# Kernel optimization log

Hardware: AMD Instinct MI355X
Metric: run time of the kernel (lower is better)

Reference implementation:

```python
import jax, jax.numpy as jnp
import numpy as np

B = 262144
NUM_PLAYERS = 450
EMBED = 8


def _lin(x, w, b):
    return x @ w + b


def setup_inputs() -> dict:
    key = jax.random.key(0)
    ks = jax.random.split(key, 32)
    # state: 73 continuous features + 5 player ids stored as floats
    cont = jax.random.normal(ks[0], (B, 73), dtype=jnp.float32)
    pids = jax.random.randint(ks[1], (B, 5), 0, NUM_PLAYERS).astype(jnp.float32)
    state = jnp.concatenate([cont, pids], axis=1)

    def w(k, shape, fan_in):
        return jax.random.normal(k, shape, dtype=jnp.float32) * (2.0 / fan_in) ** 0.5

    base_in = 13 + EMBED + 32      # ctx(21) + pooled defender phi(32) = 53
    pass_in = 32 + base_in         # tm_phi(32) + base(53) = 85? no: 32+53=85 -> wait
    pass_in = 32 + (13 + EMBED) + 32  # tm_phi + ctx + def_pooled = 32+21+32 = 85
    # Match torch: pass_input = 32 + ctx_dim + 32 where ctx_dim = 13+embed = 21 -> 85?
    # torch: ctx_dim = 13 + embed_dim = 21; base_input = ctx_dim + 32 = 53; pass_input = 32 + ctx_dim + 32 = 85.
    # BUT forward concatenates [tm_phi, ctx, def_pooled] = 32 + 21 + 32 = 85. Consistent.
    pass_in = 85
    return {
        "state": state,
        "emb": jax.random.normal(ks[2], (NUM_PLAYERS, EMBED), dtype=jnp.float32),
        "wd1": w(ks[3], (4, 32), 4),   "bd1": jnp.zeros((32,), jnp.float32),
        "wd2": w(ks[4], (32, 32), 32), "bd2": jnp.zeros((32,), jnp.float32),
        "wt1": w(ks[5], (10 + EMBED, 32), 18), "bt1": jnp.zeros((32,), jnp.float32),
        "wt2": w(ks[6], (32, 32), 32),         "bt2": jnp.zeros((32,), jnp.float32),
        "wv1": w(ks[7], (base_in, 64), base_in), "bv1": jnp.zeros((64,), jnp.float32),
        "wv2": w(ks[8], (64, 32), 64),           "bv2": jnp.zeros((32,), jnp.float32),
        "wv3": w(ks[9], (32, 1), 32),            "bv3": jnp.zeros((1,), jnp.float32),
        "ws1": w(ks[10], (base_in, 32), base_in), "bs1": jnp.zeros((32,), jnp.float32),
        "ws2": w(ks[11], (32, 1), 32),            "bs2": jnp.zeros((1,), jnp.float32),
        "wp1": w(ks[12], (pass_in, 64), pass_in), "bp1": jnp.zeros((64,), jnp.float32),
        "wp2": w(ks[13], (64, 16), 64),           "bp2": jnp.zeros((16,), jnp.float32),
        "wp3": w(ks[14], (16, 1), 16),            "bp3": jnp.zeros((1,), jnp.float32),
    }


def reference(state, emb, wd1, bd1, wd2, bd2, wt1, bt1, wt2, bt2,
              wv1, bv1, wv2, bv2, wv3, bv3, ws1, bs1, ws2, bs2,
              wp1, bp1, wp2, bp2, wp3, bp3):
    b = state.shape[0]
    context = state[:, :11]
    tm_open = state[:, 11:15]
    tm_fg = state[:, 15:19]
    tm_dist = state[:, 19:23]
    def_pos = state[:, 23:33].reshape(b, 5, 2)
    tm_pos = state[:, 33:41].reshape(b, 4, 2)
    bh_vel = state[:, 41:43]
    def_vel = state[:, 43:53].reshape(b, 5, 2)
    tm_vel = state[:, 53:61].reshape(b, 4, 2)
    tm_lane_min = state[:, 61:65]
    tm_corridor = state[:, 65:69]
    tm_pass_dist = state[:, 69:73]

    pids = jnp.clip(state[:, 73:78].astype(jnp.int32), 0, NUM_PLAYERS - 1)
    bh_embed = emb[pids[:, 0]]            # [b, E]
    tm_embeds = emb[pids[:, 1:5]]         # [b, 4, E]

    # batched defender phi over 5 entities: [b,5,4] -> [b,5,32]
    d_feat = jnp.concatenate([def_pos, def_vel], axis=-1)
    d_h = jax.nn.relu(jax.nn.relu(d_feat @ wd1 + bd1) @ wd2 + bd2)
    def_pooled = d_h.mean(axis=1)         # [b, 32]

    ctx = jnp.concatenate([context, bh_vel, bh_embed], axis=1)   # [b, 21]
    base = jnp.concatenate([ctx, def_pooled], axis=1)            # [b, 53]

    value = jax.nn.relu(jax.nn.relu(base @ wv1 + bv1) @ wv2 + bv2) @ wv3 + bv3  # [b,1]
    a_shoot = jax.nn.relu(base @ ws1 + bs1) @ ws2 + bs2                          # [b,1]

    # batched teammate phi over 4 entities: [b,4,18] -> [b,4,32]
    t_feat = jnp.concatenate([
        tm_pos, tm_vel,
        tm_open[:, :, None], tm_fg[:, :, None], tm_dist[:, :, None],
        tm_lane_min[:, :, None], tm_corridor[:, :, None], tm_pass_dist[:, :, None],
        tm_embeds,
    ], axis=-1)
    tm_phi = jax.nn.relu(jax.nn.relu(t_feat @ wt1 + bt1) @ wt2 + bt2)  # [b,4,32]

    base_b = jnp.broadcast_to(base[:, None, :], (b, 4, base.shape[1]))
    p_in = jnp.concatenate([tm_phi, base_b], axis=-1)                   # [b,4,85]
    a_pass = (jax.nn.relu(jax.nn.relu(p_in @ wp1 + bp1) @ wp2 + bp2) @ wp3 + bp3)[..., 0]  # [b,4]
    a_pass = a_pass - a_pass.mean(axis=1, keepdims=True)

    q_shoot = value + a_shoot          # [b,1]
    q_passes = value + a_pass          # [b,4]
    return jnp.concatenate([q_shoot, q_passes], axis=1)
```

## Files before the change

kernel.cpp:

```cpp
#include <hip/hip_runtime.h>
#include <hip/hip_bf16.h>

#define THREADS 512

typedef short bf16x8 __attribute__((ext_vector_type(8)));
typedef float f32x4 __attribute__((ext_vector_type(4)));

union FragU { unsigned u[4]; bf16x8 v; };

__device__ __forceinline__ void split8(const float* x, FragU& hi, FragU& lo) {
#pragma unroll
    for (int i = 0; i < 4; ++i) {
        float a = x[2 * i], b = x[2 * i + 1];
        __hip_bfloat162 h2 = __float22bfloat162_rn(make_float2(a, b));
        float ra = __bfloat162float(h2.x), rb = __bfloat162float(h2.y);
        __hip_bfloat162 l2 = __float22bfloat162_rn(make_float2(a - ra, b - rb));
        unsigned hu, lu;
        __builtin_memcpy(&hu, &h2, 4);
        __builtin_memcpy(&lu, &l2, 4);
        hi.u[i] = hu; lo.u[i] = lu;
    }
}

__device__ __forceinline__ f32x4 mm3(const FragU& ah, const FragU& al,
                                     const FragU& bh, const FragU& bl, f32x4 acc) {
    acc = __builtin_amdgcn_mfma_f32_16x16x32_bf16(al.v, bh.v, acc, 0, 0, 0);
    acc = __builtin_amdgcn_mfma_f32_16x16x32_bf16(ah.v, bl.v, acc, 0, 0, 0);
    acc = __builtin_amdgcn_mfma_f32_16x16x32_bf16(ah.v, bh.v, acc, 0, 0, 0);
    return acc;
}

__device__ __forceinline__ void load_pair(const uint4* __restrict__ ws, int pair, int lane,
                                          FragU& hi, FragU& lo) {
    uint4 a = ws[pair * 128 + lane];
    uint4 b = ws[pair * 128 + 64 + lane];
    hi.u[0] = a.x; hi.u[1] = a.y; hi.u[2] = a.z; hi.u[3] = a.w;
    lo.u[0] = b.x; lo.u[1] = b.y; lo.u[2] = b.z; lo.u[3] = b.w;
}

__device__ __forceinline__ void buildA(const float* buf, int stride, int m, int kf, int lane,
                                       FragU& hi, FragU& lo) {
    const float* p = buf + (m * 16 + (lane & 15)) * stride + kf * 32 + ((lane >> 4) * 8);
    float x[8];
    *reinterpret_cast<float4*>(&x[0]) = *reinterpret_cast<const float4*>(p);
    *reinterpret_cast<float4*>(&x[4]) = *reinterpret_cast<const float4*>(p + 4);
    split8(x, hi, lo);
}

__device__ __forceinline__ void storeC(float* buf, int stride, int m, int nf, int lane, f32x4 c) {
    float* p = buf + (((lane >> 4) * 4) + m * 16) * stride + nf * 16 + (lane & 15);
    p[0] = c[0]; p[stride] = c[1]; p[2 * stride] = c[2]; p[3 * stride] = c[3];
}

#define PB_D2  0
#define PB_T1  2
#define PB_T2  4
#define PB_P1T 6
#define PB_P1B 10
#define PB_P2  18
#define PB_V1  20
#define PB_V2  28
#define PB_S1  32
#define WS_BYTES (36 * 2048)

__global__ __launch_bounds__(64)
void prep_weights(const float* __restrict__ wd2, const float* __restrict__ wt1,
                  const float* __restrict__ wt2, const float* __restrict__ wp1,
                  const float* __restrict__ wp2, const float* __restrict__ wv1,
                  const float* __restrict__ wv2, const float* __restrict__ ws1,
                  uint4* __restrict__ wsout) {
    const int pair = blockIdx.x;
    const int lane = threadIdx.x;
    const int base_[10]  = {0, 2, 4, 6, 10, 18, 20, 28, 32, 36};
    const int kreal_[9]  = {32, 18, 32, 32, 53, 64, 53, 64, 53};
    const int n_[9]      = {32, 32, 32, 64, 64, 16, 64, 32, 32};
    const int nfc_[9]    = {2, 2, 2, 4, 4, 1, 4, 2, 2};
    const int roff_[9]   = {0, 0, 0, 0, 32, 0, 0, 0, 0};
    int g = 0;
    while (g < 8 && pair >= base_[g + 1]) ++g;
    const int local = pair - base_[g];
    const int kf = local / nfc_[g];
    const int nfi = local % nfc_[g];
    const float* W = (g == 0) ? wd2 : (g == 1) ? wt1 : (g == 2) ? wt2 :
                     (g == 3 || g == 4) ? wp1 : (g == 5) ? wp2 :
                     (g == 6) ? wv1 : (g == 7) ? wv2 : ws1;
    const int N = n_[g];
    float x[8];
#pragma unroll
    for (int j = 0; j < 8; ++j) {
        const int k = kf * 32 + (lane >> 4) * 8 + j;
        const int n = nfi * 16 + (lane & 15);
        x[j] = (k < kreal_[g]) ? W[(roff_[g] + k) * N + n] : 0.0f;
    }
    FragU hi, lo;
    split8(x, hi, lo);
    wsout[pair * 128 + lane]      = make_uint4(hi.u[0], hi.u[1], hi.u[2], hi.u[3]);
    wsout[pair * 128 + 64 + lane] = make_uint4(lo.u[0], lo.u[1], lo.u[2], lo.u[3]);
}

#define SB 68
#define SS 36
#define WAVE_F 2304

__global__ __launch_bounds__(THREADS)
void dueling_mfma(const float* __restrict__ state, const float* __restrict__ emb,
                  const float* __restrict__ wd1, const float* __restrict__ bd1,
                  const float* __restrict__ bd2, const float* __restrict__ bt1,
                  const float* __restrict__ bt2, const float* __restrict__ bv1,
                  const float* __restrict__ bv2, const float* __restrict__ wv3,
                  const float* __restrict__ bv3, const float* __restrict__ bs1,
                  const float* __restrict__ ws2, const float* __restrict__ bs2,
                  const float* __restrict__ bp1, const float* __restrict__ bp2,
                  const float* __restrict__ wp3,
                  const uint4* __restrict__ ws, float* __restrict__ out, int nrows) {
    __shared__ float smem[8 * WAVE_F];
    const int lane = threadIdx.x & 63;
    const int wave = threadIdx.x >> 6;
    const int r    = lane & 31;
    const int sub  = lane >> 5;
    const int row  = blockIdx.x * 256 + wave * 32 + r;
    const float* __restrict__ s = state + (long long)row * 78;

    float* BASE = smem + wave * WAVE_F;
    float* BUFA = BASE;
    float* BUFB = BASE + 32 * SS;
    float* HST  = BASE + 24;
    const int c16 = lane & 15;

#pragma unroll
    for (int i = 0; i < 9; ++i)
        *reinterpret_cast<float4*>(BASE + i * 256 + lane * 4) = make_float4(0.f, 0.f, 0.f, 0.f);

    if (lane < 32) {
        int pid0 = (int)s[73];
        pid0 = pid0 < 0 ? 0 : (pid0 > 449 ? 449 : pid0);
        const float4 e0 = *(const float4*)(emb + pid0 * 8);
        const float4 e1 = *(const float4*)(emb + pid0 * 8 + 4);
        float* bp = BASE + r * SB;
        *reinterpret_cast<float4*>(bp +  0) = make_float4(s[0], s[1], s[2], s[3]);
        *reinterpret_cast<float4*>(bp +  4) = make_float4(s[4], s[5], s[6], s[7]);
        *reinterpret_cast<float4*>(bp +  8) = make_float4(s[8], s[9], s[10], s[41]);
        *reinterpret_cast<float4*>(bp + 12) = make_float4(s[42], e0.x, e0.y, e0.z);
        *reinterpret_cast<float4*>(bp + 16) = make_float4(e0.w, e1.x, e1.y, e1.z);
        bp[20] = e1.w;
    }

    float pool[2][2][4];
#pragma unroll
    for (int m = 0; m < 2; ++m)
#pragma unroll
        for (int nf = 0; nf < 2; ++nf)
#pragma unroll
            for (int q = 0; q < 4; ++q) pool[m][nf][q] = 0.0f;

#pragma unroll 1
    for (int p = 0; p < 5; ++p) {
        const float f0 = s[23 + 2 * p], f1 = s[24 + 2 * p];
        const float f2 = s[43 + 2 * p], f3 = s[44 + 2 * p];
#pragma unroll
        for (int i2 = 0; i2 < 4; ++i2) {
            const int i = sub * 4 + i2;
            const float4 b4 = *(const float4*)(bd1 + i * 4);
            const float4 w0 = *(const float4*)(wd1 + 0 * 32 + i * 4);
            const float4 w1 = *(const float4*)(wd1 + 1 * 32 + i * 4);
            const float4 w2 = *(const float4*)(wd1 + 2 * 32 + i * 4);
            const float4 w3 = *(const float4*)(wd1 + 3 * 32 + i * 4);
            float4 hv;
            hv.x = fmaxf(fmaf(f0, w0.x, fmaf(f1, w1.x, fmaf(f2, w2.x, fmaf(f3, w3.x, b4.x)))), 0.f);
            hv.y = fmaxf(fmaf(f0, w0.y, fmaf(f1, w1.y, fmaf(f2, w2.y, fmaf(f3, w3.y, b4.y)))), 0.f);
            hv.z = fmaxf(fmaf(f0, w0.z, fmaf(f1, w1.z, fmaf(f2, w2.z, fmaf(f3, w3.z, b4.z)))), 0.f);
            hv.w = fmaxf(fmaf(f0, w0.w, fmaf(f1, w1.w, fmaf(f2, w2.w, fmaf(f3, w3.w, b4.w)))), 0.f);
            *reinterpret_cast<float4*>(BASE + r * SB + 24 + i * 4) = hv;
        }

        FragU ah[2], al[2];
#pragma unroll
        for (int m = 0; m < 2; ++m) buildA(HST, SB, m, 0, lane, ah[m], al[m]);
#pragma unroll
        for (int nf = 0; nf < 2; ++nf) {
            FragU bh, bl; load_pair(ws, PB_D2 + nf, lane, bh, bl);
            const float bias = bd2[nf * 16 + c16];
#pragma unroll
            for (int m = 0; m < 2; ++m) {
                f32x4 acc = {bias, bias, bias, bias};
                acc = mm3(ah[m], al[m], bh, bl, acc);
#pragma unroll
                for (int q = 0; q < 4; ++q) pool[m][nf][q] += fmaxf(acc[q], 0.0f);
            }
        }
    }
    BASE[r * SB + 53] = 0.0f;
    BASE[r * SB + 54] = 0.0f;
    BASE[r * SB + 55] = 0.0f;
#pragma unroll
    for (int m = 0; m < 2; ++m)
#pragma unroll
        for (int nf = 0; nf < 2; ++nf)
#pragma unroll
            for (int q = 0; q < 4; ++q)
                BASE[((lane >> 4) * 4 + q + m * 16) * SB + 21 + nf * 16 + c16] =
                    pool[m][nf][q] * 0.2f;

    FragU Xh[2][2], Xl[2][2];
#pragma unroll
    for (int m = 0; m < 2; ++m)
#pragma unroll
        for (int kf = 0; kf < 2; ++kf)
            buildA(BASE, SB, m, kf, lane, Xh[m][kf], Xl[m][kf]);

    float v2acc[2][2][4];
#pragma unroll
    for (int m = 0; m < 2; ++m)
#pragma unroll
        for (int nf = 0; nf < 2; ++nf) {
            const float b = bv2[nf * 16 + c16];
#pragma unroll
            for (int q = 0; q < 4; ++q) v2acc[m][nf][q] = b;
        }
#pragma unroll 1
    for (int half = 0; half < 2; ++half) {
#pragma unroll
        for (int nfl = 0; nfl < 2; ++nfl) {
            const int ng = half * 2 + nfl;
            FragU b0h, b0l, b1h, b1l;
            load_pair(ws, PB_V1 + ng, lane, b0h, b0l);
            load_pair(ws, PB_V1 + 4 + ng, lane, b1h, b1l);
            const float bias = bv1[ng * 16 + c16];
#pragma unroll
            for (int m = 0; m < 2; ++m) {
                f32x4 acc = {bias, bias, bias, bias};
                acc = mm3(Xh[m][0], Xl[m][0], b0h, b0l, acc);
                acc = mm3(Xh[m][1], Xl[m][1], b1h, b1l, acc);
#pragma unroll
                for (int q = 0; q < 4; ++q) acc[q] = fmaxf(acc[q], 0.0f);
                storeC(BUFA, SS, m, nfl, lane, acc);
            }
        }
        FragU ah[2], al[2];
#pragma unroll
        for (int m = 0; m < 2; ++m) buildA(BUFA, SS, m, 0, lane, ah[m], al[m]);
#pragma unroll
        for (int nf = 0; nf < 2; ++nf) {
            FragU bh, bl; load_pair(ws, PB_V2 + half * 2 + nf, lane, bh, bl);
#pragma unroll
            for (int m = 0; m < 2; ++m) {
                f32x4 acc = {v2acc[m][nf][0], v2acc[m][nf][1], v2acc[m][nf][2], v2acc[m][nf][3]};
                acc = mm3(ah[m], al[m], bh, bl, acc);
#pragma unroll
                for (int q = 0; q < 4; ++q) v2acc[m][nf][q] = acc[q];
            }
        }
    }
#pragma unroll
    for (int m = 0; m < 2; ++m)
#pragma unroll
        for (int nf = 0; nf < 2; ++nf) {
            f32x4 rr = {fmaxf(v2acc[m][nf][0], 0.f), fmaxf(v2acc[m][nf][1], 0.f),
                        fmaxf(v2acc[m][nf][2], 0.f), fmaxf(v2acc[m][nf][3], 0.f)};
            storeC(BUFA, SS, m, nf, lane, rr);
        }
    float value = bv3[0];
#pragma unroll
    for (int c4 = 0; c4 < 8; ++c4) {
        float4 v = *reinterpret_cast<const float4*>(BUFA + r * SS + c4 * 4);
        value = fmaf(v.x, wv3[c4 * 4], value);
        value = fmaf(v.y, wv3[c4 * 4 + 1], value);
        value = fmaf(v.z, wv3[c4 * 4 + 2], value);
        value = fmaf(v.w, wv3[c4 * 4 + 3], value);
    }

#pragma unroll
    for (int nf = 0; nf < 2; ++nf) {
        FragU b0h, b0l, b1h, b1l;
        load_pair(ws, PB_S1 + nf, lane, b0h, b0l);
        load_pair(ws, PB_S1 + 2 + nf, lane, b1h, b1l);
        const float bias = bs1[nf * 16 + c16];
#pragma unroll
        for (int m = 0; m < 2; ++m) {
            f32x4 acc = {bias, bias, bias, bias};
            acc = mm3(Xh[m][0], Xl[m][0], b0h, b0l, acc);
            acc = mm3(Xh[m][1], Xl[m][1], b1h, b1l, acc);
#pragma unroll
            for (int q = 0; q < 4; ++q) acc[q] = fmaxf(acc[q], 0.0f);
            storeC(BUFA, SS, m, nf, lane, acc);
        }
    }
    float ashoot = bs2[0];
#pragma unroll
    for (int c4 = 0; c4 < 8; ++c4) {
        float4 v = *reinterpret_cast<const float4*>(BUFA + r * SS + c4 * 4);
        ashoot = fmaf(v.x, ws2[c4 * 4], ashoot);
        ashoot = fmaf(v.y, ws2[c4 * 4 + 1], ashoot);
        ashoot = fmaf(v.z, ws2[c4 * 4 + 2], ashoot);
        ashoot = fmaf(v.w, ws2[c4 * 4 + 3], ashoot);
    }

    float ap0 = 0.f, ap1 = 0.f, ap2 = 0.f, ap3 = 0.f;
#pragma unroll 1
    for (int j = 0; j < 4; ++j) {
        if (lane < 32) {
            int pid = (int)s[74 + j];
            pid = pid < 0 ? 0 : (pid > 449 ? 449 : pid);
            const float4 e0 = *(const float4*)(emb + pid * 8);
            const float4 e1 = *(const float4*)(emb + pid * 8 + 4);
            float* tp = BUFA + r * SS;
            *reinterpret_cast<float4*>(tp +  0) =
                make_float4(s[33 + 2 * j], s[34 + 2 * j], s[53 + 2 * j], s[54 + 2 * j]);
            *reinterpret_cast<float4*>(tp +  4) =
                make_float4(s[11 + j], s[15 + j], s[19 + j], s[61 + j]);
            *reinterpret_cast<float4*>(tp +  8) = make_float4(s[65 + j], s[69 + j], e0.x, e0.y);
            *reinterpret_cast<float4*>(tp + 12) = make_float4(e0.z, e0.w, e1.x, e1.y);
            *reinterpret_cast<float4*>(tp + 16) = make_float4(e1.z, e1.w, 0.f, 0.f);
            *reinterpret_cast<float4*>(tp + 20) = make_float4(0.f, 0.f, 0.f, 0.f);
            *reinterpret_cast<float4*>(tp + 24) = make_float4(0.f, 0.f, 0.f, 0.f);
            *reinterpret_cast<float4*>(tp + 28) = make_float4(0.f, 0.f, 0.f, 0.f);
        }
        {
            FragU ah[2], al[2];
#pragma unroll
            for (int m = 0; m < 2; ++m) buildA(BUFA, SS, m, 0, lane, ah[m], al[m]);
#pragma unroll
            for (int nf = 0; nf < 2; ++nf) {
                FragU bh, bl; load_pair(ws, PB_T1 + nf, lane, bh, bl);
                const float bias = bt1[nf * 16 + c16];
#pragma unroll
                for (int m = 0; m < 2; ++m) {
                    f32x4 acc = {bias, bias, bias, bias};
                    acc = mm3(ah[m], al[m], bh, bl, acc);
#pragma unroll
                    for (int q = 0; q < 4; ++q) acc[q] = fmaxf(acc[q], 0.0f);
                    storeC(BUFB, SS, m, nf, lane, acc);
                }
            }
        }
        {
            FragU ah[2], al[2];
#pragma unroll
            for (int m = 0; m < 2; ++m) buildA(BUFB, SS, m, 0, lane, ah[m], al[m]);
#pragma unroll
            for (int nf = 0; nf < 2; ++nf) {
                FragU bh, bl; load_pair(ws, PB_T2 + nf, lane, bh, bl);
                const float bias = bt2[nf * 16 + c16];
#pragma unroll
                for (int m = 0; m < 2; ++m) {
                    f32x4 acc = {bias, bias, bias, bias};
                    acc = mm3(ah[m], al[m], bh, bl, acc);
#pragma unroll
                    for (int q = 0; q < 4; ++q) acc[q] = fmaxf(acc[q], 0.0f);
                    storeC(BUFA, SS, m, nf, lane, acc);
                }
            }
        }
        FragU th[2], tl[2];
#pragma unroll
        for (int m = 0; m < 2; ++m) buildA(BUFA, SS, m, 0, lane, th[m], tl[m]);

        float p2acc[2][4];
        {
            const float b = bp2[c16];
#pragma unroll
            for (int m = 0; m < 2; ++m)
#pragma unroll
                for (int q = 0; q < 4; ++q) p2acc[m][q] = b;
        }
#pragma unroll 1
        for (int half = 0; half < 2; ++half) {
#pragma unroll
            for (int nfl = 0; nfl < 2; ++nfl) {
                const int ng = half * 2 + nfl;
                FragU bth, btl, b0h, b0l, b1h, b1l;
                load_pair(ws, PB_P1T + ng, lane, bth, btl);
                load_pair(ws, PB_P1B + ng, lane, b0h, b0l);
                load_pair(ws, PB_P1B + 4 + ng, lane, b1h, b1l);
                const float bias = bp1[ng * 16 + c16];
#pragma unroll
                for (int m = 0; m < 2; ++m) {
                    f32x4 acc = {bias, bias, bias, bias};
                    acc = mm3(th[m], tl[m], bth, btl, acc);
                    acc = mm3(Xh[m][0], Xl[m][0], b0h, b0l, acc);
                    acc = mm3(Xh[m][1], Xl[m][1], b1h, b1l, acc);
#pragma unroll
                    for (int q = 0; q < 4; ++q) acc[q] = fmaxf(acc[q], 0.0f);
                    storeC(BUFB, SS, m, nfl, lane, acc);
                }
            }
            FragU ah[2], al[2];
#pragma unroll
            for (int m = 0; m < 2; ++m) buildA(BUFB, SS, m, 0, lane, ah[m], al[m]);
            FragU bh, bl; load_pair(ws, PB_P2 + half, lane, bh, bl);
#pragma unroll
            for (int m = 0; m < 2; ++m) {
                f32x4 acc = {p2acc[m][0], p2acc[m][1], p2acc[m][2], p2acc[m][3]};
                acc = mm3(ah[m], al[m], bh, bl, acc);
#pragma unroll
                for (int q = 0; q < 4; ++q) p2acc[m][q] = acc[q];
            }
        }
#pragma unroll
        for (int m = 0; m < 2; ++m) {
            f32x4 rr = {fmaxf(p2acc[m][0], 0.f), fmaxf(p2acc[m][1], 0.f),
                        fmaxf(p2acc[m][2], 0.f), fmaxf(p2acc[m][3], 0.f)};
            storeC(BUFB, SS, m, 0, lane, rr);
        }
        float ap = 0.0f;
#pragma unroll
        for (int c4 = 0; c4 < 4; ++c4) {
            float4 v = *reinterpret_cast<const float4*>(BUFB + r * SS + c4 * 4);
            ap = fmaf(v.x, wp3[c4 * 4], ap);
            ap = fmaf(v.y, wp3[c4 * 4 + 1], ap);
            ap = fmaf(v.z, wp3[c4 * 4 + 2], ap);
            ap = fmaf(v.w, wp3[c4 * 4 + 3], ap);
        }
        if (j == 0) ap0 = ap;
        else if (j == 1) ap1 = ap;
        else if (j == 2) ap2 = ap;
        else ap3 = ap;
    }

    if (lane < 32) {
        const float am = 0.25f * (ap0 + ap1 + ap2 + ap3);
        float* __restrict__ o = out + (long long)row * 5;
        o[0] = value + ashoot;
        o[1] = value + ap0 - am;
        o[2] = value + ap1 - am;
        o[3] = value + ap2 - am;
        o[4] = value + ap3 - am;
    }
}

__global__ __launch_bounds__(256)
void dueling_fwd_valu(const float* __restrict__ state, const float* __restrict__ emb,
                      const float* __restrict__ wd1, const float* __restrict__ bd1,
                      const float* __restrict__ wd2, const float* __restrict__ bd2,
                      const float* __restrict__ wt1, const float* __restrict__ bt1,
                      const float* __restrict__ wt2, const float* __restrict__ bt2,
                      const float* __restrict__ wv1, const float* __restrict__ bv1,
                      const float* __restrict__ wv2, const float* __restrict__ bv2,
                      const float* __restrict__ wv3, const float* __restrict__ bv3,
                      const float* __restrict__ ws1, const float* __restrict__ bs1,
                      const float* __restrict__ ws2, const float* __restrict__ bs2,
                      const float* __restrict__ wp1, const float* __restrict__ bp1,
                      const float* __restrict__ wp2, const float* __restrict__ bp2,
                      const float* __restrict__ wp3, const float* __restrict__ bp3,
                      float* __restrict__ out, int nrows) {
    const int row = blockIdx.x * 256 + threadIdx.x;
    if (row >= nrows) return;
    const float* __restrict__ s = state + (long long)row * 78;
    float def_pooled[32];
#pragma unroll
    for (int n = 0; n < 32; ++n) def_pooled[n] = 0.0f;
#pragma unroll 1
    for (int p = 0; p < 5; ++p) {
        const float f0 = s[23 + 2 * p], f1 = s[24 + 2 * p], f2 = s[43 + 2 * p], f3 = s[44 + 2 * p];
        float h1[32];
#pragma unroll
        for (int n = 0; n < 32; ++n) {
            float a = bd1[n];
            a = fmaf(f0, wd1[n], a); a = fmaf(f1, wd1[32 + n], a);
            a = fmaf(f2, wd1[64 + n], a); a = fmaf(f3, wd1[96 + n], a);
            h1[n] = fmaxf(a, 0.0f);
        }
        float a2[32];
#pragma unroll
        for (int n = 0; n < 32; ++n) a2[n] = bd2[n];
#pragma unroll
        for (int k = 0; k < 32; ++k) {
            const float hk = h1[k];
#pragma unroll
            for (int n = 0; n < 32; ++n) a2[n] = fmaf(hk, wd2[k * 32 + n], a2[n]);
        }
#pragma unroll
        for (int n = 0; n < 32; ++n) def_pooled[n] += fmaxf(a2[n], 0.0f);
    }
    float base[53];
#pragma unroll
    for (int i = 0; i < 11; ++i) base[i] = s[i];
    base[11] = s[41]; base[12] = s[42];
    {
        int pid0 = (int)s[73];
        pid0 = pid0 < 0 ? 0 : (pid0 > 449 ? 449 : pid0);
        const float4 e0 = *(const float4*)(emb + pid0 * 8);
        const float4 e1 = *(const float4*)(emb + pid0 * 8 + 4);
        base[13] = e0.x; base[14] = e0.y; base[15] = e0.z; base[16] = e0.w;
        base[17] = e1.x; base[18] = e1.y; base[19] = e1.z; base[20] = e1.w;
    }
#pragma unroll
    for (int n = 0; n < 32; ++n) base[21 + n] = def_pooled[n] * 0.2f;
    float a_shoot;
    {
        float t[32];
#pragma unroll
        for (int n = 0; n < 32; ++n) t[n] = bs1[n];
#pragma unroll
        for (int k = 0; k < 53; ++k) {
            const float xk = base[k];
#pragma unroll
            for (int n = 0; n < 32; ++n) t[n] = fmaf(xk, ws1[k * 32 + n], t[n]);
        }
        a_shoot = bs2[0];
#pragma unroll
        for (int k = 0; k < 32; ++k) a_shoot = fmaf(fmaxf(t[k], 0.0f), ws2[k], a_shoot);
    }
    float value;
    {
        float h32[32];
#pragma unroll
        for (int n = 0; n < 32; ++n) h32[n] = bv2[n];
#pragma unroll
        for (int half = 0; half < 2; ++half) {
            float hh[32];
#pragma unroll
            for (int n = 0; n < 32; ++n) hh[n] = bv1[half * 32 + n];
#pragma unroll
            for (int k = 0; k < 53; ++k) {
                const float xk = base[k];
#pragma unroll
                for (int n = 0; n < 32; ++n) hh[n] = fmaf(xk, wv1[k * 64 + half * 32 + n], hh[n]);
            }
#pragma unroll
            for (int k = 0; k < 32; ++k) {
                const float xk = fmaxf(hh[k], 0.0f);
#pragma unroll
                for (int n = 0; n < 32; ++n) h32[n] = fmaf(xk, wv2[(half * 32 + k) * 32 + n], h32[n]);
            }
        }
        value = bv3[0];
#pragma unroll
        for (int k = 0; k < 32; ++k) value = fmaf(fmaxf(h32[k], 0.0f), wv3[k], value);
    }
    float pb[64];
#pragma unroll
    for (int n = 0; n < 64; ++n) pb[n] = bp1[n];
#pragma unroll
    for (int k = 0; k < 53; ++k) {
        const float xk = base[k];
#pragma unroll
        for (int n = 0; n < 64; ++n) pb[n] = fmaf(xk, wp1[(32 + k) * 64 + n], pb[n]);
    }
    float ap0 = 0.f, ap1 = 0.f, ap2 = 0.f, ap3 = 0.f;
#pragma unroll 1
    for (int j = 0; j < 4; ++j) {
        float t1[32];
        {
            float tf[18];
            tf[0] = s[33 + 2 * j]; tf[1] = s[34 + 2 * j];
            tf[2] = s[53 + 2 * j]; tf[3] = s[54 + 2 * j];
            tf[4] = s[11 + j]; tf[5] = s[15 + j]; tf[6] = s[19 + j];
            tf[7] = s[61 + j]; tf[8] = s[65 + j]; tf[9] = s[69 + j];
            int pid = (int)s[74 + j];
            pid = pid < 0 ? 0 : (pid > 449 ? 449 : pid);
            const float4 e0 = *(const float4*)(emb + pid * 8);
            const float4 e1 = *(const float4*)(emb + pid * 8 + 4);
            tf[10] = e0.x; tf[11] = e0.y; tf[12] = e0.z; tf[13] = e0.w;
            tf[14] = e1.x; tf[15] = e1.y; tf[16] = e1.z; tf[17] = e1.w;
#pragma unroll
            for (int n = 0; n < 32; ++n) t1[n] = bt1[n];
#pragma unroll
            for (int k = 0; k < 18; ++k) {
                const float xk = tf[k];
#pragma unroll
                for (int n = 0; n < 32; ++n) t1[n] = fmaf(xk, wt1[k * 32 + n], t1[n]);
            }
        }
        float t2[32];
#pragma unroll
        for (int n = 0; n < 32; ++n) t2[n] = bt2[n];
#pragma unroll
        for (int k = 0; k < 32; ++k) {
            const float xk = fmaxf(t1[k], 0.0f);
#pragma unroll
            for (int n = 0; n < 32; ++n) t2[n] = fmaf(xk, wt2[k * 32 + n], t2[n]);
        }
#pragma unroll
        for (int n = 0; n < 32; ++n) t2[n] = fmaxf(t2[n], 0.0f);
        float p2[16];
#pragma unroll
        for (int n = 0; n < 16; ++n) p2[n] = bp2[n];
#pragma unroll
        for (int half = 0; half < 2; ++half) {
            float phh[32];
#pragma unroll
            for (int n = 0; n < 32; ++n) phh[n] = pb[half * 32 + n];
#pragma unroll
            for (int k = 0; k < 32; ++k) {
                const float xk = t2[k];
#pragma unroll
                for (int n = 0; n < 32; ++n) phh[n] = fmaf(xk, wp1[k * 64 + half * 32 + n], phh[n]);
            }
#pragma unroll
            for (int k = 0; k < 32; ++k) {
                const float xk = fmaxf(phh[k], 0.0f);
#pragma unroll
                for (int n = 0; n < 16; ++n) p2[n] = fmaf(xk, wp2[(half * 32 + k) * 16 + n], p2[n]);
            }
        }
        float a = bp3[0];
#pragma unroll
        for (int k = 0; k < 16; ++k) a = fmaf(fmaxf(p2[k], 0.0f), wp3[k], a);
        if (j == 0) ap0 = a; else if (j == 1) ap1 = a; else if (j == 2) ap2 = a; else ap3 = a;
    }
    const float am = 0.25f * (ap0 + ap1 + ap2 + ap3);
    float* __restrict__ o = out + (long long)row * 5;
    o[0] = value + a_shoot;
    o[1] = value + ap0 - am;
    o[2] = value + ap1 - am;
    o[3] = value + ap2 - am;
    o[4] = value + ap3 - am;
}

extern "C" void kernel_launch(void* const* d_in, const int* in_sizes, int n_in,
                              void* d_out, int out_size, void* d_ws, size_t ws_size,
                              hipStream_t stream) {
    const float* state = (const float*)d_in[0];
    const float* emb   = (const float*)d_in[1];
    const float* wd1 = (const float*)d_in[2];  const float* bd1 = (const float*)d_in[3];
    const float* wd2 = (const float*)d_in[4];  const float* bd2 = (const float*)d_in[5];
    const float* wt1 = (const float*)d_in[6];  const float* bt1 = (const float*)d_in[7];
    const float* wt2 = (const float*)d_in[8];  const float* bt2 = (const float*)d_in[9];
    const float* wv1 = (const float*)d_in[10]; const float* bv1 = (const float*)d_in[11];
    const float* wv2 = (const float*)d_in[12]; const float* bv2 = (const float*)d_in[13];
    const float* wv3 = (const float*)d_in[14]; const float* bv3 = (const float*)d_in[15];
    const float* ws1 = (const float*)d_in[16]; const float* bs1 = (const float*)d_in[17];
    const float* ws2 = (const float*)d_in[18]; const float* bs2 = (const float*)d_in[19];
    const float* wp1 = (const float*)d_in[20]; const float* bp1 = (const float*)d_in[21];
    const float* wp2 = (const float*)d_in[22]; const float* bp2 = (const float*)d_in[23];
    const float* wp3 = (const float*)d_in[24]; const float* bp3 = (const float*)d_in[25];

    const int nrows = in_sizes[0] / 78;

    if (ws_size < (size_t)WS_BYTES || (nrows & 255) != 0) {
        const int blocks = (nrows + 255) / 256;
        dueling_fwd_valu<<<blocks, 256, 0, stream>>>(
            state, emb, wd1, bd1, wd2, bd2, wt1, bt1, wt2, bt2,
            wv1, bv1, wv2, bv2, wv3, bv3, ws1, bs1, ws2, bs2,
            wp1, bp1, wp2, bp2, wp3, bp3, (float*)d_out, nrows);
        return;
    }

    prep_weights<<<36, 64, 0, stream>>>(wd2, wt1, wt2, wp1, wp2, wv1, wv2, ws1,
                                        (uint4*)d_ws);
    dueling_mfma<<<nrows / 256, THREADS, 0, stream>>>(
        state, emb, wd1, bd1, bd2, bt1, bt2, bv1, bv2, wv3, bv3,
        bs1, ws2, bs2, bp1, bp2, wp3,
        (const uint4*)d_ws, (float*)d_out, nrows);
}
```

Baseline: 128.0 us.

## Process two teammates per loop iteration to reuse weight fragments

The teammate loop now handles two teammates per iteration. Both lane halves gather inputs, one teammate each, instead of half the lanes idling. Each loaded weight fragment pair is reused across both teammates' MFMAs, which halves weight loads and loop overhead and exposes more independent MFMA work. The cost is double the per-wave shared memory (about 147KB per block, which limits occupancy) and more live registers for the doubled fragments and accumulators.

```diff
diff --git a/kernel.cpp b/kernel.cpp
--- a/kernel.cpp
+++ b/kernel.cpp
@@ -100,7 +100,7 @@
 
 #define SB 68
 #define SS 36
-#define WAVE_F 2304
+#define WAVE_F 4608
 
 __global__ __launch_bounds__(THREADS)
 void dueling_mfma(const float* __restrict__ state, const float* __restrict__ emb,
@@ -121,15 +121,20 @@
     const int row  = blockIdx.x * 256 + wave * 32 + r;
     const float* __restrict__ s = state + (long long)row * 78;
 
-    float* BASE = smem + wave * WAVE_F;
-    float* BUFA = BASE;
-    float* BUFB = BASE + 32 * SS;
-    float* HST  = BASE + 24;
+    float* REG0 = smem + wave * WAVE_F;
+    float* BASE = REG0;
+    float* HST  = REG0 + 24;
+    float* BUFA = REG0;
+    float* BUFB = REG0 + 1152;
+    float* TA0  = REG0;
+    float* TB0  = REG0 + 1152;
+    float* TA1  = REG0 + 2304;
+    float* TB1  = REG0 + 3456;
     const int c16 = lane & 15;
 
 #pragma unroll
-    for (int i = 0; i < 9; ++i)
-        *reinterpret_cast<float4*>(BASE + i * 256 + lane * 4) = make_float4(0.f, 0.f, 0.f, 0.f);
+    for (int i = 0; i < 18; ++i)
+        *reinterpret_cast<float4*>(REG0 + i * 256 + lane * 4) = make_float4(0.f, 0.f, 0.f, 0.f);
 
     if (lane < 32) {
         int pid0 = (int)s[73];
@@ -297,18 +302,19 @@
 
     float ap0 = 0.f, ap1 = 0.f, ap2 = 0.f, ap3 = 0.f;
 #pragma unroll 1
-    for (int j = 0; j < 4; ++j) {
-        if (lane < 32) {
-            int pid = (int)s[74 + j];
+    for (int jj = 0; jj < 4; jj += 2) {
+        {
+            const int jme = jj + sub;
+            int pid = (int)s[74 + jme];
             pid = pid < 0 ? 0 : (pid > 449 ? 449 : pid);
             const float4 e0 = *(const float4*)(emb + pid * 8);
             const float4 e1 = *(const float4*)(emb + pid * 8 + 4);
-            float* tp = BUFA + r * SS;
+            float* tp = (sub ? TA1 : TA0) + r * SS;
             *reinterpret_cast<float4*>(tp +  0) =
-                make_float4(s[33 + 2 * j], s[34 + 2 * j], s[53 + 2 * j], s[54 + 2 * j]);
+                make_float4(s[33 + 2 * jme], s[34 + 2 * jme], s[53 + 2 * jme], s[54 + 2 * jme]);
             *reinterpret_cast<float4*>(tp +  4) =
-                make_float4(s[11 + j], s[15 + j], s[19 + j], s[61 + j]);
-            *reinterpret_cast<float4*>(tp +  8) = make_float4(s[65 + j], s[69 + j], e0.x, e0.y);
+                make_float4(s[11 + jme], s[15 + jme], s[19 + jme], s[61 + jme]);
+            *reinterpret_cast<float4*>(tp +  8) = make_float4(s[65 + jme], s[69 + jme], e0.x, e0.y);
             *reinterpret_cast<float4*>(tp + 12) = make_float4(e0.z, e0.w, e1.x, e1.y);
             *reinterpret_cast<float4*>(tp + 16) = make_float4(e1.z, e1.w, 0.f, 0.f);
             *reinterpret_cast<float4*>(tp + 20) = make_float4(0.f, 0.f, 0.f, 0.f);
@@ -316,52 +322,67 @@
             *reinterpret_cast<float4*>(tp + 28) = make_float4(0.f, 0.f, 0.f, 0.f);
         }
         {
-            FragU ah[2], al[2];
-#pragma unroll
-            for (int m = 0; m < 2; ++m) buildA(BUFA, SS, m, 0, lane, ah[m], al[m]);
+            FragU ah[2][2], al[2][2];
+#pragma unroll
+            for (int b = 0; b < 2; ++b)
+#pragma unroll
+                for (int m = 0; m < 2; ++m)
+                    buildA(b ? TA1 : TA0, SS, m, 0, lane, ah[b][m], al[b][m]);
 #pragma unroll
             for (int nf = 0; nf < 2; ++nf) {
                 FragU bh, bl; load_pair(ws, PB_T1 + nf, lane, bh, bl);
                 const float bias = bt1[nf * 16 + c16];
 #pragma unroll
-                for (int m = 0; m < 2; ++m) {
-                    f32x4 acc = {bias, bias, bias, bias};
-                    acc = mm3(ah[m], al[m], bh, bl, acc);
-#pragma unroll
-                    for (int q = 0; q < 4; ++q) acc[q] = fmaxf(acc[q], 0.0f);
-                    storeC(BUFB, SS, m, nf, lane, acc);
-                }
+                for (int b = 0; b < 2; ++b)
+#pragma unroll
+                    for (int m = 0; m < 2; ++m) {
+                        f32x4 acc = {bias, bias, bias, bias};
+                        acc = mm3(ah[b][m], al[b][m], bh, bl, acc);
+#pragma unroll
+                        for (int q = 0; q < 4; ++q) acc[q] = fmaxf(acc[q], 0.0f);
+                        storeC(b ? TB1 : TB0, SS, m, nf, lane, acc);
+                    }
             }
         }
         {
-            FragU ah[2], al[2];
-#pragma unroll
-            for (int m = 0; m < 2; ++m) buildA(BUFB, SS, m, 0, lane, ah[m], al[m]);
+            FragU ah[2][2], al[2][2];
+#pragma unroll
+            for (int b = 0; b < 2; ++b)
+#pragma unroll
+                for (int m = 0; m < 2; ++m)
+                    buildA(b ? TB1 : TB0, SS, m, 0, lane, ah[b][m], al[b][m]);
 #pragma unroll
             for (int nf = 0; nf < 2; ++nf) {
                 FragU bh, bl; load_pair(ws, PB_T2 + nf, lane, bh, bl);
                 const float bias = bt2[nf * 16 + c16];
 #pragma unroll
-                for (int m = 0; m < 2; ++m) {
-                    f32x4 acc = {bias, bias, bias, bias};
-                    acc = mm3(ah[m], al[m], bh, bl, acc);
-#pragma unroll
-                    for (int q = 0; q < 4; ++q) acc[q] = fmaxf(acc[q], 0.0f);
-                    storeC(BUFA, SS, m, nf, lane, acc);
-                }
-            }
-        }
-        FragU th[2], tl[2];
-#pragma unroll
-        for (int m = 0; m < 2; ++m) buildA(BUFA, SS, m, 0, lane, th[m], tl[m]);
-
-        float p2acc[2][4];
+                for (int b = 0; b < 2; ++b)
+#pragma unroll
+                    for (int m = 0; m < 2; ++m) {
+                        f32x4 acc = {bias, bias, bias, bias};
+                        acc = mm3(ah[b][m], al[b][m], bh, bl, acc);
+#pragma unroll
+                        for (int q = 0; q < 4; ++q) acc[q] = fmaxf(acc[q], 0.0f);
+                        storeC(b ? TA1 : TA0, SS, m, nf, lane, acc);
+                    }
+            }
+        }
+        FragU th[2][2], tl_[2][2];
+#pragma unroll
+        for (int b = 0; b < 2; ++b)
+#pragma unroll
+            for (int m = 0; m < 2; ++m)
+                buildA(b ? TA1 : TA0, SS, m, 0, lane, th[b][m], tl_[b][m]);
+
+        float p2acc[2][2][4];
         {
-            const float b = bp2[c16];
-#pragma unroll
-            for (int m = 0; m < 2; ++m)
-#pragma unroll
-                for (int q = 0; q < 4; ++q) p2acc[m][q] = b;
+            const float bq = bp2[c16];
+#pragma unroll
+            for (int b = 0; b < 2; ++b)
+#pragma unroll
+                for (int m = 0; m < 2; ++m)
+#pragma unroll
+                    for (int q = 0; q < 4; ++q) p2acc[b][m][q] = bq;
         }
 #pragma unroll 1
         for (int half = 0; half < 2; ++half) {
@@ -374,47 +395,53 @@
                 load_pair(ws, PB_P1B + 4 + ng, lane, b1h, b1l);
                 const float bias = bp1[ng * 16 + c16];
 #pragma unroll
+                for (int b = 0; b < 2; ++b)
+#pragma unroll
+                    for (int m = 0; m < 2; ++m) {
+                        f32x4 acc = {bias, bias, bias, bias};
+                        acc = mm3(th[b][m], tl_[b][m], bth, btl, acc);
+                        acc = mm3(Xh[m][0], Xl[m][0], b0h, b0l, acc);
+                        acc = mm3(Xh[m][1], Xl[m][1], b1h, b1l, acc);
+#pragma unroll
+                        for (int q = 0; q < 4; ++q) acc[q] = fmaxf(acc[q], 0.0f);
+                        storeC(b ? TB1 : TB0, SS, m, nfl, lane, acc);
+                    }
+            }
+            FragU bh, bl; load_pair(ws, PB_P2 + half, lane, bh, bl);
+#pragma unroll
+            for (int b = 0; b < 2; ++b)
+#pragma unroll
                 for (int m = 0; m < 2; ++m) {
-                    f32x4 acc = {bias, bias, bias, bias};
-                    acc = mm3(th[m], tl[m], bth, btl, acc);
-                    acc = mm3(Xh[m][0], Xl[m][0], b0h, b0l, acc);
-                    acc = mm3(Xh[m][1], Xl[m][1], b1h, b1l, acc);
-#pragma unroll
-                    for (int q = 0; q < 4; ++q) acc[q] = fmaxf(acc[q], 0.0f);
-                    storeC(BUFB, SS, m, nfl, lane, acc);
+                    FragU ah, al; buildA(b ? TB1 : TB0, SS, m, 0, lane, ah, al);
+                    f32x4 acc = {p2acc[b][m][0], p2acc[b][m][1], p2acc[b][m][2], p2acc[b][m][3]};
+                    acc = mm3(ah, al, bh, bl, acc);
+#pragma unroll
+                    for (int q = 0; q < 4; ++q) p2acc[b][m][q] = acc[q];
                 }
-            }
-            FragU ah[2], al[2];
-#pragma unroll
-            for (int m = 0; m < 2; ++m) buildA(BUFB, SS, m, 0, lane, ah[m], al[m]);
-            FragU bh, bl; load_pair(ws, PB_P2 + half, lane, bh, bl);
+        }
+        float apj[2];
+#pragma unroll
+        for (int b = 0; b < 2; ++b) {
 #pragma unroll
             for (int m = 0; m < 2; ++m) {
-                f32x4 acc = {p2acc[m][0], p2acc[m][1], p2acc[m][2], p2acc[m][3]};
-                acc = mm3(ah[m], al[m], bh, bl, acc);
-#pragma unroll
-                for (int q = 0; q < 4; ++q) p2acc[m][q] = acc[q];
-            }
-        }
-#pragma unroll
-        for (int m = 0; m < 2; ++m) {
-            f32x4 rr = {fmaxf(p2acc[m][0], 0.f), fmaxf(p2acc[m][1], 0.f),
-                        fmaxf(p2acc[m][2], 0.f), fmaxf(p2acc[m][3], 0.f)};
-            storeC(BUFB, SS, m, 0, lane, rr);
-        }
-        float ap = 0.0f;
-#pragma unroll
-        for (int c4 = 0; c4 < 4; ++c4) {
-            float4 v = *reinterpret_cast<const float4*>(BUFB + r * SS + c4 * 4);
-            ap = fmaf(v.x, wp3[c4 * 4], ap);
-            ap = fmaf(v.y, wp3[c4 * 4 + 1], ap);
-            ap = fmaf(v.z, wp3[c4 * 4 + 2], ap);
-            ap = fmaf(v.w, wp3[c4 * 4 + 3], ap);
-        }
-        if (j == 0) ap0 = ap;
-        else if (j == 1) ap1 = ap;
-        else if (j == 2) ap2 = ap;
-        else ap3 = ap;
+                f32x4 rr = {fmaxf(p2acc[b][m][0], 0.f), fmaxf(p2acc[b][m][1], 0.f),
+                            fmaxf(p2acc[b][m][2], 0.f), fmaxf(p2acc[b][m][3], 0.f)};
+                storeC(b ? TB1 : TB0, SS, m, 0, lane, rr);
+            }
+            float ap = 0.0f;
+            const float* tb = (b ? TB1 : TB0) + r * SS;
+#pragma unroll
+            for (int c4 = 0; c4 < 4; ++c4) {
+                float4 v = *reinterpret_cast<const float4*>(tb + c4 * 4);
+                ap = fmaf(v.x, wp3[c4 * 4], ap);
+                ap = fmaf(v.y, wp3[c4 * 4 + 1], ap);
+                ap = fmaf(v.z, wp3[c4 * 4 + 2], ap);
+                ap = fmaf(v.w, wp3[c4 * 4 + 3], ap);
+            }
+            apj[b] = ap;
+        }
+        if (jj == 0) { ap0 = apj[0]; ap1 = apj[1]; }
+        else         { ap2 = apj[0]; ap3 = apj[1]; }
     }
 
     if (lane < 32) {
```

After: 128.2 us. Within noise of the previous version (+0.1%).
